# Kernel tuning notes

Hardware: AMD Instinct MI355X
Metric: run time of the kernel (lower is better)

The kernel has to match this reference:

```python
import jax, jax.numpy as jnp
import numpy as np

N, E, B = 50000, 800000, 1000
NODE_DIN, BB_DOUT, DHID, K = 32, 64, 64, 3
GLOB_DIN, EMBED_DIN = 64, 64
CIN = BB_DOUT + NODE_DIN  # 96


def setup_inputs() -> dict:
    key = jax.random.key(0)
    ks = jax.random.split(key, 24)

    def w(k, shape, fan_in):
        return jax.random.normal(k, shape, jnp.float32) / np.float32(np.sqrt(fan_in))

    inp = dict(
        x=jax.random.normal(ks[0], (N, NODE_DIN), jnp.float32),
        u=jax.random.normal(ks[1], (B, GLOB_DIN), jnp.float32),
        z=jax.random.normal(ks[2], (N, BB_DOUT), jnp.float32),
        edge_index=jax.random.randint(ks[3], (2, E), 0, N),
        edge_weight=jax.random.uniform(ks[4], (E,), jnp.float32),
        batch=jnp.sort(jax.random.randint(ks[5], (N,), 0, B)),
        batch_size=B,
        prev_h=jax.random.normal(ks[6], (N, DHID), jnp.float32),
    )
    # six ChebConvs of GConvGRU: x-convs take CIN, h-convs take DHID; all output DHID
    for i, nm in enumerate(["xz", "hz", "xr", "hr", "xh", "hh"]):
        cin = CIN if nm[0] == "x" else DHID
        inp[f"W{nm}"] = w(ks[7 + 2 * i], (K, cin, DHID), cin * K)
        inp[f"b{nm}"] = jnp.zeros((DHID,), jnp.float32)
    inp["Wg"] = w(ks[20], (GLOB_DIN, EMBED_DIN), GLOB_DIN)
    inp["bg"] = jnp.zeros((EMBED_DIN,), jnp.float32)
    return inp


def _cheb(xin, W, b, src, dst, w_norm, n):
    """ChebConv with sym norm, lambda_max=2 -> L_hat = -D^-1/2 A D^-1/2 (diag cancels)."""
    def prop(t):  # L_hat @ t  ([N,C])
        return -jax.ops.segment_sum(w_norm[:, None] * t[src], dst, num_segments=n)

    out = xin @ W[0] + b
    tx_prev = xin
    tx = None
    if W.shape[0] > 1:
        tx = prop(xin)
        out = out + tx @ W[1]
    for k in range(2, W.shape[0]):
        tx_new = 2.0 * prop(tx) - tx_prev
        out = out + tx_new @ W[k]
        tx_prev, tx = tx, tx_new
    return out


def reference(x, u, z, edge_index, edge_weight, batch, batch_size, prev_h,
              Wxz, bxz, Whz, bhz, Wxr, bxr, Whr, bhr, Wxh, bxh, Whh, bhh, Wg, bg):
    n = x.shape[0]
    src, dst = edge_index[0], edge_index[1]
    deg = jax.ops.segment_sum(edge_weight, src, num_segments=n)
    deg_safe = jnp.where(deg > 0, deg, 1.0)
    dinv = jnp.where(deg > 0, jax.lax.rsqrt(deg_safe), 0.0)
    w_norm = dinv[src] * edge_weight * dinv[dst]

    xin = jnp.concatenate([z, x], axis=-1)  # [N, CIN]
    Z = jax.nn.sigmoid(_cheb(xin, Wxz, bxz, src, dst, w_norm, n)
                       + _cheb(prev_h, Whz, bhz, src, dst, w_norm, n))
    R = jax.nn.sigmoid(_cheb(xin, Wxr, bxr, src, dst, w_norm, n)
                       + _cheb(prev_h, Whr, bhr, src, dst, w_norm, n))
    Ht = jnp.tanh(_cheb(xin, Wxh, bxh, src, dst, w_norm, n)
                  + _cheb(prev_h * R, Whh, bhh, src, dst, w_norm, n))
    h = Z * prev_h + (1.0 - Z) * Ht

    graph_emb = jax.ops.segment_sum(z, batch, num_segments=batch_size)  # [B, BB_DOUT]
    global_emb = jax.nn.relu(u @ Wg + bg)                                # [B, EMBED_DIN]
    fused = jnp.concatenate([graph_emb, global_emb], axis=-1)           # [B, 128]
    return fused, h
```

## Files before the change

### kernel.cpp

```cpp
#include <hip/hip_runtime.h>

#define NN 50000
#define EE 800000
#define BB 1000
#define NB 196
#define NR 8
#define RS 6272
#define NC 32
#define CHUNK 25000

#define DEGBLKS (NR * NC)
#define BUILDBLKS 15625
#define PACKBLKS 204

typedef unsigned short u16;
typedef __attribute__((ext_vector_type(8))) short bf16x8;
typedef __attribute__((ext_vector_type(4))) float f32x4;

static __device__ __forceinline__ u16 f2b(float f) {
    union { float f; unsigned u; } v;
    v.f = f;
    unsigned r = v.u + 0x7fffu + ((v.u >> 16) & 1u);
    return (u16)(r >> 16);
}

static __device__ __forceinline__ float b2f(short s) {
    union { unsigned u; float f; } c;
    c.u = ((unsigned)(u16)s) << 16;
    return c.f;
}

__global__ __launch_bounds__(512) void k_front(
    const int* __restrict__ src, const int* __restrict__ dst,
    const float* __restrict__ ew, float* __restrict__ deg_p, int* __restrict__ cnt_p,
    const float* __restrict__ z, const float* __restrict__ x,
    const float* __restrict__ ph, u16* __restrict__ A,
    const float* __restrict__ Wxz, const float* __restrict__ Wxr,
    const float* __restrict__ Wxh, const float* __restrict__ Whz,
    const float* __restrict__ Whr, const float* __restrict__ Whh,
    u16* __restrict__ Wp, u16* __restrict__ W3p, int* __restrict__ ctr) {
    __shared__ float sdeg[RS];
    __shared__ int scnt[RS];
    int bid = blockIdx.x;
    if (bid < DEGBLKS) {
        if (bid == 0 && threadIdx.x == 0) atomicExch(ctr, 0);
        int r = bid & (NR - 1);
        int c = bid >> 3;
        int base = r * RS;
        for (int i = threadIdx.x; i < RS; i += 512) {
            sdeg[i] = 0.f;
            scnt[i] = 0;
        }
        __syncthreads();
        int e0 = c * CHUNK;
        for (int j = threadIdx.x; j < CHUNK; j += 512) {
            int e = e0 + j;
            int s = src[e], d = dst[e];
            int sl = s - base, dl = d - base;
            if ((unsigned)sl < RS) atomicAdd(&sdeg[sl], ew[e]);
            if ((unsigned)dl < RS) atomicAdd(&scnt[dl], 1);
        }
        __syncthreads();
        int lim = (NN - base < RS) ? (NN - base) : RS;
        for (int i = threadIdx.x; i < lim; i += 512) {
            deg_p[(size_t)c * NN + base + i] = sdeg[i];
            cnt_p[(size_t)c * NN + base + i] = scnt[i];
        }
    } else if (bid < DEGBLKS + BUILDBLKS) {
        int i = (bid - DEGBLKS) * 512 + threadIdx.x;
        int n = i / 160, c = i - n * 160;
        float v;
        if (c < 64) v = z[n * 64 + c];
        else if (c < 96) v = x[n * 32 + (c - 64)];
        else v = ph[n * 64 + (c - 96)];
        A[(size_t)n * 480 + c] = f2b(v);
    } else {
        int idx = (bid - DEGBLKS - BUILDBLKS) * 512 + threadIdx.x;
        if (idx < 15 * 12 * 512) {
            int j = idx & 7, l = (idx >> 3) & 63;
            int ct = (idx >> 9) % 12, s = (idx >> 9) / 12;
            int k = 32 * s + (l >> 4) * 8 + j;
            int g = ct >> 2;
            int c = 16 * (ct & 3) + (l & 15);
            bool isX;
            int kr;
            if (k < 96)       { isX = true;  kr = k; }
            else if (k < 160) { isX = false; kr = k - 96; }
            else if (k < 256) { isX = true;  kr = 96 + (k - 160); }
            else if (k < 320) { isX = false; kr = 64 + (k - 256); }
            else if (k < 416) { isX = true;  kr = 192 + (k - 320); }
            else              { isX = false; kr = 128 + (k - 416); }
            float val;
            if (isX) {
                const float* W = (g == 0) ? Wxz : ((g == 1) ? Wxr : Wxh);
                val = W[kr * 64 + c];
            } else if (g == 2) {
                val = 0.f;
            } else {
                const float* W = (g == 0) ? Whz : Whr;
                val = W[kr * 64 + c];
            }
            Wp[idx] = f2b(val);
        } else {
            int i2 = idx - 15 * 12 * 512;
            int j = i2 & 7, l = (i2 >> 3) & 63;
            int ct = (i2 >> 9) & 3, s = i2 >> 11;
            int k = 32 * s + (l >> 4) * 8 + j;
            int ki = k >> 6, kr = k & 63;
            int c = 16 * ct + (l & 15);
            W3p[i2] = f2b(Whh[(ki * 64 + kr) * 64 + c]);
        }
    }
}

__global__ __launch_bounds__(256) void k_scan(
    const int* __restrict__ cnt_p, const float* __restrict__ deg_p,
    int* __restrict__ cnt, int* __restrict__ row_ptr, int* __restrict__ cursor,
    float* __restrict__ dinv, int* __restrict__ bsum, int* __restrict__ ctr) {
    __shared__ int s[256];
    int b = blockIdx.x;
    int i = b * 256 + threadIdx.x;
    int v = 0;
    float d = 0.f;
    if (i < NN) {
#pragma unroll
        for (int p = 0; p < NC; p++) v += cnt_p[(size_t)p * NN + i];
#pragma unroll
        for (int p = 0; p < NC; p++) d += deg_p[(size_t)p * NN + i];
        cnt[i] = v;
    }
    s[threadIdx.x] = v;
    __syncthreads();
    for (int off = 1; off < 256; off <<= 1) {
        int t = (threadIdx.x >= off) ? s[threadIdx.x - off] : 0;
        __syncthreads();
        s[threadIdx.x] += t;
        __syncthreads();
    }
    int incl = s[threadIdx.x];
    if (threadIdx.x == 255) atomicExch(&bsum[b], s[255]);
    __threadfence();
    if (threadIdx.x == 0) {
        atomicAdd(ctr, 1);
        while (atomicAdd(ctr, 0) < NB) __builtin_amdgcn_s_sleep(8);
    }
    __syncthreads();
    __threadfence();
    int pv = (threadIdx.x < b) ? atomicAdd(&bsum[threadIdx.x], 0) : 0;
    s[threadIdx.x] = pv;
    __syncthreads();
    for (int off = 128; off > 0; off >>= 1) {
        if (threadIdx.x < off) s[threadIdx.x] += s[threadIdx.x + off];
        __syncthreads();
    }
    int prefix = s[0];
    if (i < NN) {
        int start = prefix + incl - v;
        row_ptr[i] = start;
        cursor[i] = start;
        dinv[i] = d > 0.f ? rsqrtf(d) : 0.f;
    }
}

__global__ void k_scatter(const int* __restrict__ src, const int* __restrict__ dst,
                          const float* __restrict__ ew, const float* __restrict__ dinv,
                          int* __restrict__ cursor, uint2* __restrict__ csr8) {
    int e = blockIdx.x * 256 + threadIdx.x;
    if (e >= EE) return;
    int d = dst[e], s = src[e];
    int pos = atomicAdd(&cursor[d], 1);
    float w = dinv[s] * ew[e] * dinv[d];
    csr8[pos] = make_uint2((unsigned)s, __float_as_uint(w));
}

template <int C, int SCALE, bool HB, int BS, int OS>
__global__ __launch_bounds__(BS) void k_pull(
    const u16* __restrict__ Abase, int inofs, int baseofs, int outofs,
    const uint2* __restrict__ csr8, const int* __restrict__ row_ptr,
    const int* __restrict__ cnt) {
    constexpr int TPR = C / 16;
    int tid = blockIdx.x * BS + threadIdx.x;
    int r = tid / TPR;
    int c16 = (tid - r * TPR) * 16;
    if (r >= NN) return;
    int s0 = row_ptr[r], n = cnt[r];
    float acc[16];
#pragma unroll
    for (int k = 0; k < 16; k++) acc[k] = 0.f;
    const u16* in = Abase + inofs + c16;
    uint2 e = (n > 0) ? csr8[s0] : make_uint2(0u, 0u);
    for (int j = 0; j < n; j++) {
        uint2 ec = e;
        if (j + 1 < n) e = csr8[s0 + j + 1];
        float w = __uint_as_float(ec.y);
        const u16* p = in + (size_t)ec.x * OS;
        bf16x8 v0 = *(const bf16x8*)(p);
        bf16x8 v1 = *(const bf16x8*)(p + 8);
#pragma unroll
        for (int k = 0; k < 8; k++) {
            acc[k] += w * b2f(v0[k]);
            acc[8 + k] += w * b2f(v1[k]);
        }
    }
    const float sc = -(float)SCALE;
    float o[16];
    if (HB) {
        const u16* bp = Abase + (size_t)r * OS + baseofs + c16;
        bf16x8 b0 = *(const bf16x8*)(bp);
        bf16x8 b1 = *(const bf16x8*)(bp + 8);
#pragma unroll
        for (int k = 0; k < 8; k++) {
            o[k] = sc * acc[k] - b2f(b0[k]);
            o[8 + k] = sc * acc[8 + k] - b2f(b1[k]);
        }
    } else {
#pragma unroll
        for (int k = 0; k < 16; k++) o[k] = sc * acc[k];
    }
    bf16x8 p0, p1;
#pragma unroll
    for (int k = 0; k < 8; k++) {
        p0[k] = (short)f2b(o[k]);
        p1[k] = (short)f2b(o[8 + k]);
    }
    u16* op = const_cast<u16*>(Abase) + (size_t)r * OS + outofs + c16;
    *(bf16x8*)(op) = p0;
    *(bf16x8*)(op + 8) = p1;
}

__global__ __launch_bounds__(256) void k_gates_mfma(
    const u16* __restrict__ A, const u16* __restrict__ Wp,
    const float* __restrict__ bxz, const float* __restrict__ bhz,
    const float* __restrict__ bxr, const float* __restrict__ bhr,
    const float* __restrict__ bxh,
    u16* __restrict__ Zb16, u16* __restrict__ Hx16, u16* __restrict__ A3) {
    int wv = (blockIdx.x * 256 + threadIdx.x) >> 6;
    int lane = threadIdx.x & 63;
    int r0 = wv * 16;
    if (r0 >= NN) return;
    int q = lane >> 4, j0 = lane & 15;

    f32x4 acc[12];
#pragma unroll
    for (int i = 0; i < 12; i++) acc[i] = (f32x4){0.f, 0.f, 0.f, 0.f};

    const u16* arow = A + (size_t)(r0 + j0) * 480 + q * 8;
#pragma unroll
    for (int s = 0; s < 15; s++) {
        bf16x8 a = *(const bf16x8*)(arow + 32 * s);
        const u16* bp = Wp + (size_t)(s * 12) * 512 + lane * 8;
#pragma unroll
        for (int ct = 0; ct < 12; ct++) {
            bf16x8 b = *(const bf16x8*)(bp + ct * 512);
            acc[ct] = __builtin_amdgcn_mfma_f32_16x16x32_bf16(a, b, acc[ct], 0, 0, 0);
        }
    }

#pragma unroll
    for (int ct = 0; ct < 4; ct++) {
        int j = 16 * ct + j0;
        float bz = bxz[j] + bhz[j];
        float br = bxr[j] + bhr[j];
        float bh = bxh[j];
#pragma unroll
        for (int reg = 0; reg < 4; reg++) {
            int r = r0 + q * 4 + reg;
            size_t i = (size_t)r * 64 + j;
            float zp = acc[ct][reg] + bz;
            float rp = acc[ct + 4][reg] + br;
            float hp = acc[ct + 8][reg] + bh;
            float zv = 1.f / (1.f + expf(-zp));
            float rv = 1.f / (1.f + expf(-rp));
            float phv = b2f((short)A[(size_t)r * 480 + 96 + j]);
            Zb16[i] = f2b(zv);
            Hx16[i] = f2b(hp);
            A3[(size_t)r * 192 + j] = f2b(rv * phv);
        }
    }
}

#define FINBLKS 782
__global__ __launch_bounds__(256) void k_final_tail(
    const u16* __restrict__ A3, const u16* __restrict__ W3p,
    const float* __restrict__ bhh, const u16* __restrict__ Hx16,
    const u16* __restrict__ Zb16, const u16* __restrict__ A,
    float* __restrict__ outh,
    const float* __restrict__ z, const int* __restrict__ batch,
    const float* __restrict__ u, const float* __restrict__ Wg,
    const float* __restrict__ bg, float* __restrict__ outF) {
    if (blockIdx.x >= FINBLKS) {
        int b = ((blockIdx.x - FINBLKS) * 256 + threadIdx.x) >> 6;
        int lane = threadIdx.x & 63;
        if (b >= BB) return;
        int lo = 0, hi = NN;
        while (lo < hi) {
            int m = (lo + hi) >> 1;
            if (batch[m] < b) lo = m + 1; else hi = m;
        }
        int start = lo;
        hi = NN;
        while (lo < hi) {
            int m = (lo + hi) >> 1;
            if (batch[m] < b + 1) lo = m + 1; else hi = m;
        }
        int end = lo;
        float acc = 0.f;
        for (int n = start; n < end; n++) acc += z[(size_t)n * 64 + lane];
        float g = bg[lane];
        const float* ur = u + (size_t)b * 64;
        for (int k = 0; k < 64; k++) g += ur[k] * Wg[k * 64 + lane];
        g = fmaxf(g, 0.f);
        outF[(size_t)b * 128 + lane] = acc;
        outF[(size_t)b * 128 + 64 + lane] = g;
        return;
    }
    int wv = (blockIdx.x * 256 + threadIdx.x) >> 6;
    int lane = threadIdx.x & 63;
    int r0 = wv * 16;
    if (r0 >= NN) return;
    int q = lane >> 4, j0 = lane & 15;

    f32x4 acc[4];
#pragma unroll
    for (int i = 0; i < 4; i++) acc[i] = (f32x4){0.f, 0.f, 0.f, 0.f};

    const u16* arow = A3 + (size_t)(r0 + j0) * 192 + q * 8;
#pragma unroll
    for (int s = 0; s < 6; s++) {
        bf16x8 a = *(const bf16x8*)(arow + 32 * s);
        const u16* bp = W3p + (size_t)(s * 4) * 512 + lane * 8;
#pragma unroll
        for (int ct = 0; ct < 4; ct++) {
            bf16x8 b = *(const bf16x8*)(bp + ct * 512);
            acc[ct] = __builtin_amdgcn_mfma_f32_16x16x32_bf16(a, b, acc[ct], 0, 0, 0);
        }
    }

#pragma unroll
    for (int ct = 0; ct < 4; ct++) {
        int j = 16 * ct + j0;
        float bh = bhh[j];
#pragma unroll
        for (int reg = 0; reg < 4; reg++) {
            int r = r0 + q * 4 + reg;
            size_t i = (size_t)r * 64 + j;
            float ht = tanhf(b2f((short)Hx16[i]) + acc[ct][reg] + bh);
            float zv = b2f((short)Zb16[i]);
            float phv = b2f((short)A[(size_t)r * 480 + 96 + j]);
            outh[i] = zv * phv + (1.f - zv) * ht;
        }
    }
}

extern "C" void kernel_launch(void* const* d_in, const int* in_sizes, int n_in,
                              void* d_out, int out_size, void* d_ws, size_t ws_size,
                              hipStream_t stream) {
    const float* x  = (const float*)d_in[0];
    const float* u  = (const float*)d_in[1];
    const float* z  = (const float*)d_in[2];
    const int*   ei = (const int*)d_in[3];
    const float* ew = (const float*)d_in[4];
    const int* batch = (const int*)d_in[5];
    const float* ph = (const float*)d_in[7];
    const float *Wxz = (const float*)d_in[8],  *bxz = (const float*)d_in[9];
    const float *Whz = (const float*)d_in[10], *bhz = (const float*)d_in[11];
    const float *Wxr = (const float*)d_in[12], *bxr = (const float*)d_in[13];
    const float *Whr = (const float*)d_in[14], *bhr = (const float*)d_in[15];
    const float *Wxh = (const float*)d_in[16], *bxh = (const float*)d_in[17];
    const float *Whh = (const float*)d_in[18], *bhh = (const float*)d_in[19];
    const float *Wg  = (const float*)d_in[20], *bg  = (const float*)d_in[21];
    const int* src = ei;
    const int* dst = ei + EE;

    char* wsb = (char*)d_ws;
    size_t o = 0;
    auto alloc = [&](size_t bytes) {
        void* p = wsb + o;
        o += (bytes + 255) & ~(size_t)255;
        return p;
    };
    float* deg_p   = (float*)alloc((size_t)NC * NN * 4);
    int*   cnt_p   = (int*)alloc((size_t)NC * NN * 4);
    int*   cnt     = (int*)alloc(NN * 4);
    int*   row_ptr = (int*)alloc(NN * 4);
    int*   cursor  = (int*)alloc(NN * 4);
    float* dinv    = (float*)alloc(NN * 4);
    int*   bsum    = (int*)alloc(256 * 4);
    int*   ctr     = (int*)alloc(256);
    uint2* csr8    = (uint2*)alloc((size_t)EE * 8);
    u16*   Zb16 = (u16*)alloc((size_t)NN * 64 * 2);
    u16*   Hx16 = (u16*)alloc((size_t)NN * 64 * 2);
    u16*   A    = (u16*)alloc((size_t)NN * 480 * 2);
    u16*   A3   = (u16*)alloc((size_t)NN * 192 * 2);
    u16*   Wp   = (u16*)alloc(15 * 12 * 512 * 2);
    u16*   W3p  = (u16*)alloc(6 * 4 * 512 * 2);

    float* outF = (float*)d_out;
    float* outH = outF + (size_t)BB * 128;

    const int BLK = 256;
    const int gE = (EE + BLK - 1) / BLK;
    const int gPull160 = (NN + 31) / 32;
    const int gPull64 = (NN + 63) / 64;
    const int gMFMA = FINBLKS;
    const int gTail = (BB * 64 + BLK - 1) / BLK;

    k_front<<<DEGBLKS + BUILDBLKS + PACKBLKS, 512, 0, stream>>>(
        src, dst, ew, deg_p, cnt_p, z, x, ph, A,
        Wxz, Wxr, Wxh, Whz, Whr, Whh, Wp, W3p, ctr);

    k_scan<<<NB, 256, 0, stream>>>(cnt_p, deg_p, cnt, row_ptr, cursor, dinv, bsum, ctr);

    k_scatter<<<gE, BLK, 0, stream>>>(src, dst, ew, dinv, cursor, csr8);

    k_pull<160, 1, false, 320, 480><<<gPull160, 320, 0, stream>>>(A, 0, 0, 160, csr8, row_ptr, cnt);
    k_pull<160, 2, true, 320, 480><<<gPull160, 320, 0, stream>>>(A, 160, 0, 320, csr8, row_ptr, cnt);

    k_gates_mfma<<<gMFMA, BLK, 0, stream>>>(A, Wp, bxz, bhz, bxr, bhr, bxh, Zb16, Hx16, A3);

    k_pull<64, 1, false, 256, 192><<<gPull64, 256, 0, stream>>>(A3, 0, 0, 64, csr8, row_ptr, cnt);
    k_pull<64, 2, true, 256, 192><<<gPull64, 256, 0, stream>>>(A3, 64, 0, 128, csr8, row_ptr, cnt);

    k_final_tail<<<gMFMA + gTail, BLK, 0, stream>>>(A3, W3p, bhh, Hx16, Zb16, A, outH,
                                                    z, batch, u, Wg, bg, outF);
}
```

Measured before the change: 426.6 us.

## Replace atomic CSR scatter with per-chunk rank scatter and split A buffer

The CSR build no longer uses global atomic cursors. A histogram pass packs 16-bit destination counts in shared memory over 5 row ranges. The scan now also produces per-chunk base offsets, and a new scatter kernel ranks edges with shared-memory atomics and writes them deterministically. The interleaved 480-wide A buffer is split into three 160-wide buffers, and the feature/weight packing moves into the scan launch. The aim is to cut global atomic contention during the scatter, at the cost of a 32xN cbase array and a second pass over the edges.

```diff
diff --git a/kernel.cpp b/kernel.cpp
--- a/kernel.cpp
+++ b/kernel.cpp
@@ -4,14 +4,14 @@
 #define EE 800000
 #define BB 1000
 #define NB 196
-#define NR 8
-#define RS 6272
+#define NR 5
+#define RS 10496
 #define NC 32
 #define CHUNK 25000
 
-#define DEGBLKS (NR * NC)
-#define BUILDBLKS 15625
-#define PACKBLKS 204
+#define BUILD2 31250
+#define PACK2 408
+#define FINBLKS 782
 
 typedef unsigned short u16;
 typedef __attribute__((ext_vector_type(8))) short bf16x8;
@@ -30,93 +30,87 @@
     return c.f;
 }
 
-__global__ __launch_bounds__(512) void k_front(
+__global__ __launch_bounds__(512) void k_hist(
     const int* __restrict__ src, const int* __restrict__ dst,
-    const float* __restrict__ ew, float* __restrict__ deg_p, int* __restrict__ cnt_p,
+    const float* __restrict__ ew, float* __restrict__ deg_p,
+    int* __restrict__ cnt_p, int* __restrict__ ctr) {
+    __shared__ float sdeg[RS];
+    __shared__ unsigned scnt2[RS / 2];
+    if (blockIdx.x == 0 && threadIdx.x == 0) atomicExch(ctr, 0);
+    int r = blockIdx.x % NR;
+    int c = blockIdx.x / NR;
+    int base = r * RS;
+    for (int i = threadIdx.x; i < RS; i += 512) sdeg[i] = 0.f;
+    for (int i = threadIdx.x; i < RS / 2; i += 512) scnt2[i] = 0u;
+    __syncthreads();
+    int e0 = c * CHUNK;
+    for (int j = threadIdx.x; j < CHUNK; j += 512) {
+        int e = e0 + j;
+        int s = src[e], d = dst[e];
+        int sl = s - base, dl = d - base;
+        if ((unsigned)sl < RS) atomicAdd(&sdeg[sl], ew[e]);
+        if ((unsigned)dl < RS) atomicAdd(&scnt2[dl >> 1], (dl & 1) ? 65536u : 1u);
+    }
+    __syncthreads();
+    int lim = (NN - base < RS) ? (NN - base) : RS;
+    for (int i = threadIdx.x; i < lim; i += 512) {
+        deg_p[(size_t)c * NN + base + i] = sdeg[i];
+        cnt_p[(size_t)c * NN + base + i] = (int)((scnt2[i >> 1] >> ((i & 1) * 16)) & 0xffffu);
+    }
+}
+
+__global__ __launch_bounds__(256) void k_scan_build(
+    const int* __restrict__ cnt_p, const float* __restrict__ deg_p,
+    int* __restrict__ cnt, int* __restrict__ cbase, float* __restrict__ dinv,
+    int* __restrict__ bsum, int* __restrict__ ctr,
     const float* __restrict__ z, const float* __restrict__ x,
-    const float* __restrict__ ph, u16* __restrict__ A,
+    const float* __restrict__ ph, u16* __restrict__ A0,
     const float* __restrict__ Wxz, const float* __restrict__ Wxr,
     const float* __restrict__ Wxh, const float* __restrict__ Whz,
     const float* __restrict__ Whr, const float* __restrict__ Whh,
-    u16* __restrict__ Wp, u16* __restrict__ W3p, int* __restrict__ ctr) {
-    __shared__ float sdeg[RS];
-    __shared__ int scnt[RS];
-    int bid = blockIdx.x;
-    if (bid < DEGBLKS) {
-        if (bid == 0 && threadIdx.x == 0) atomicExch(ctr, 0);
-        int r = bid & (NR - 1);
-        int c = bid >> 3;
-        int base = r * RS;
-        for (int i = threadIdx.x; i < RS; i += 512) {
-            sdeg[i] = 0.f;
-            scnt[i] = 0;
-        }
-        __syncthreads();
-        int e0 = c * CHUNK;
-        for (int j = threadIdx.x; j < CHUNK; j += 512) {
-            int e = e0 + j;
-            int s = src[e], d = dst[e];
-            int sl = s - base, dl = d - base;
-            if ((unsigned)sl < RS) atomicAdd(&sdeg[sl], ew[e]);
-            if ((unsigned)dl < RS) atomicAdd(&scnt[dl], 1);
-        }
-        __syncthreads();
-        int lim = (NN - base < RS) ? (NN - base) : RS;
-        for (int i = threadIdx.x; i < lim; i += 512) {
-            deg_p[(size_t)c * NN + base + i] = sdeg[i];
-            cnt_p[(size_t)c * NN + base + i] = scnt[i];
-        }
-    } else if (bid < DEGBLKS + BUILDBLKS) {
-        int i = (bid - DEGBLKS) * 512 + threadIdx.x;
-        int n = i / 160, c = i - n * 160;
-        float v;
-        if (c < 64) v = z[n * 64 + c];
-        else if (c < 96) v = x[n * 32 + (c - 64)];
-        else v = ph[n * 64 + (c - 96)];
-        A[(size_t)n * 480 + c] = f2b(v);
-    } else {
-        int idx = (bid - DEGBLKS - BUILDBLKS) * 512 + threadIdx.x;
-        if (idx < 15 * 12 * 512) {
-            int j = idx & 7, l = (idx >> 3) & 63;
-            int ct = (idx >> 9) % 12, s = (idx >> 9) / 12;
-            int k = 32 * s + (l >> 4) * 8 + j;
-            int g = ct >> 2;
-            int c = 16 * (ct & 3) + (l & 15);
-            bool isX;
-            int kr;
-            if (k < 96)       { isX = true;  kr = k; }
-            else if (k < 160) { isX = false; kr = k - 96; }
-            else if (k < 256) { isX = true;  kr = 96 + (k - 160); }
-            else if (k < 320) { isX = false; kr = 64 + (k - 256); }
-            else if (k < 416) { isX = true;  kr = 192 + (k - 320); }
-            else              { isX = false; kr = 128 + (k - 416); }
-            float val;
-            if (isX) {
-                const float* W = (g == 0) ? Wxz : ((g == 1) ? Wxr : Wxh);
-                val = W[kr * 64 + c];
-            } else if (g == 2) {
-                val = 0.f;
+    u16* __restrict__ Wp, u16* __restrict__ W3p) {
+    if (blockIdx.x >= NB) {
+        int bid = blockIdx.x - NB;
+        if (bid < BUILD2) {
+            int i = bid * 256 + threadIdx.x;
+            int n = i / 160, c = i - n * 160;
+            float v;
+            if (c < 64) v = z[n * 64 + c];
+            else if (c < 96) v = x[n * 32 + (c - 64)];
+            else v = ph[n * 64 + (c - 96)];
+            A0[(size_t)n * 160 + c] = f2b(v);
+        } else {
+            int idx = (bid - BUILD2) * 256 + threadIdx.x;
+            if (idx < 15 * 12 * 512) {
+                int j = idx & 7, l = (idx >> 3) & 63;
+                int ct = (idx >> 9) % 12, s = (idx >> 9) / 12;
+                int k = 32 * s + (l >> 4) * 8 + j;
+                int g = ct >> 2;
+                int c = 16 * (ct & 3) + (l & 15);
+                int lvl = k / 160, kk = k - lvl * 160;
+                float val;
+                if (kk < 96) {
+                    const float* W = (g == 0) ? Wxz : ((g == 1) ? Wxr : Wxh);
+                    val = W[(lvl * 96 + kk) * 64 + c];
+                } else if (g == 2) {
+                    val = 0.f;
+                } else {
+                    const float* W = (g == 0) ? Whz : Whr;
+                    val = W[(lvl * 64 + (kk - 96)) * 64 + c];
+                }
+                Wp[idx] = f2b(val);
             } else {
-                const float* W = (g == 0) ? Whz : Whr;
-                val = W[kr * 64 + c];
+                int i2 = idx - 15 * 12 * 512;
+                int j = i2 & 7, l = (i2 >> 3) & 63;
+                int ct = (i2 >> 9) & 3, s = i2 >> 11;
+                int k = 32 * s + (l >> 4) * 8 + j;
+                int ki = k >> 6, kr = k & 63;
+                int c = 16 * ct + (l & 15);
+                W3p[i2] = f2b(Whh[(ki * 64 + kr) * 64 + c]);
             }
-            Wp[idx] = f2b(val);
-        } else {
-            int i2 = idx - 15 * 12 * 512;
-            int j = i2 & 7, l = (i2 >> 3) & 63;
-            int ct = (i2 >> 9) & 3, s = i2 >> 11;
-            int k = 32 * s + (l >> 4) * 8 + j;
-            int ki = k >> 6, kr = k & 63;
-            int c = 16 * ct + (l & 15);
-            W3p[i2] = f2b(Whh[(ki * 64 + kr) * 64 + c]);
-        }
-    }
-}
-
-__global__ __launch_bounds__(256) void k_scan(
-    const int* __restrict__ cnt_p, const float* __restrict__ deg_p,
-    int* __restrict__ cnt, int* __restrict__ row_ptr, int* __restrict__ cursor,
-    float* __restrict__ dinv, int* __restrict__ bsum, int* __restrict__ ctr) {
+        }
+        return;
+    }
     __shared__ int s[256];
     int b = blockIdx.x;
     int i = b * 256 + threadIdx.x;
@@ -155,27 +149,45 @@
     }
     int prefix = s[0];
     if (i < NN) {
-        int start = prefix + incl - v;
-        row_ptr[i] = start;
-        cursor[i] = start;
+        int run = prefix + incl - v;
         dinv[i] = d > 0.f ? rsqrtf(d) : 0.f;
-    }
-}
-
-__global__ void k_scatter(const int* __restrict__ src, const int* __restrict__ dst,
-                          const float* __restrict__ ew, const float* __restrict__ dinv,
-                          int* __restrict__ cursor, uint2* __restrict__ csr8) {
-    int e = blockIdx.x * 256 + threadIdx.x;
-    if (e >= EE) return;
-    int d = dst[e], s = src[e];
-    int pos = atomicAdd(&cursor[d], 1);
-    float w = dinv[s] * ew[e] * dinv[d];
-    csr8[pos] = make_uint2((unsigned)s, __float_as_uint(w));
-}
-
-template <int C, int SCALE, bool HB, int BS, int OS>
+#pragma unroll
+        for (int c = 0; c < NC; c++) {
+            cbase[(size_t)c * NN + i] = run;
+            run += cnt_p[(size_t)c * NN + i];
+        }
+    }
+}
+
+__global__ __launch_bounds__(512) void k_scatter_rank(
+    const int* __restrict__ src, const int* __restrict__ dst,
+    const float* __restrict__ ew, const float* __restrict__ dinv,
+    const int* __restrict__ cbase, uint2* __restrict__ csr8) {
+    __shared__ unsigned rank2[RS / 2];
+    int r = blockIdx.x % NR;
+    int c = blockIdx.x / NR;
+    int base = r * RS;
+    for (int i = threadIdx.x; i < RS / 2; i += 512) rank2[i] = 0u;
+    __syncthreads();
+    int e0 = c * CHUNK;
+    for (int j = threadIdx.x; j < CHUNK; j += 512) {
+        int e = e0 + j;
+        int d = dst[e];
+        int dl = d - base;
+        if ((unsigned)dl < RS) {
+            int s = src[e];
+            unsigned old = atomicAdd(&rank2[dl >> 1], (dl & 1) ? 65536u : 1u);
+            int rank = (int)((old >> ((dl & 1) * 16)) & 0xffffu);
+            int pos = cbase[(size_t)c * NN + d] + rank;
+            float w = dinv[s] * ew[e] * dinv[d];
+            csr8[pos] = make_uint2((unsigned)s, __float_as_uint(w));
+        }
+    }
+}
+
+template <int C, int SCALE, bool HB, int BS, int INS, int OUTS>
 __global__ __launch_bounds__(BS) void k_pull(
-    const u16* __restrict__ Abase, int inofs, int baseofs, int outofs,
+    const u16* __restrict__ in, const u16* __restrict__ base, u16* __restrict__ out,
     const uint2* __restrict__ csr8, const int* __restrict__ row_ptr,
     const int* __restrict__ cnt) {
     constexpr int TPR = C / 16;
@@ -187,13 +199,13 @@
     float acc[16];
 #pragma unroll
     for (int k = 0; k < 16; k++) acc[k] = 0.f;
-    const u16* in = Abase + inofs + c16;
+    const u16* inp = in + c16;
     uint2 e = (n > 0) ? csr8[s0] : make_uint2(0u, 0u);
     for (int j = 0; j < n; j++) {
         uint2 ec = e;
         if (j + 1 < n) e = csr8[s0 + j + 1];
         float w = __uint_as_float(ec.y);
-        const u16* p = in + (size_t)ec.x * OS;
+        const u16* p = inp + (size_t)ec.x * INS;
         bf16x8 v0 = *(const bf16x8*)(p);
         bf16x8 v1 = *(const bf16x8*)(p + 8);
 #pragma unroll
@@ -205,7 +217,7 @@
     const float sc = -(float)SCALE;
     float o[16];
     if (HB) {
-        const u16* bp = Abase + (size_t)r * OS + baseofs + c16;
+        const u16* bp = base + (size_t)r * INS + c16;
         bf16x8 b0 = *(const bf16x8*)(bp);
         bf16x8 b1 = *(const bf16x8*)(bp + 8);
 #pragma unroll
@@ -223,13 +235,14 @@
         p0[k] = (short)f2b(o[k]);
         p1[k] = (short)f2b(o[8 + k]);
     }
-    u16* op = const_cast<u16*>(Abase) + (size_t)r * OS + outofs + c16;
+    u16* op = out + (size_t)r * OUTS + c16;
     *(bf16x8*)(op) = p0;
     *(bf16x8*)(op + 8) = p1;
 }
 
 __global__ __launch_bounds__(256) void k_gates_mfma(
-    const u16* __restrict__ A, const u16* __restrict__ Wp,
+    const u16* __restrict__ A0, const u16* __restrict__ A1, const u16* __restrict__ A2,
+    const u16* __restrict__ Wp,
     const float* __restrict__ bxz, const float* __restrict__ bhz,
     const float* __restrict__ bxr, const float* __restrict__ bhr,
     const float* __restrict__ bxh,
@@ -244,10 +257,11 @@
 #pragma unroll
     for (int i = 0; i < 12; i++) acc[i] = (f32x4){0.f, 0.f, 0.f, 0.f};
 
-    const u16* arow = A + (size_t)(r0 + j0) * 480 + q * 8;
+    size_t rofs = (size_t)(r0 + j0) * 160 + q * 8;
+    const u16* arow[3] = {A0 + rofs, A1 + rofs, A2 + rofs};
 #pragma unroll
     for (int s = 0; s < 15; s++) {
-        bf16x8 a = *(const bf16x8*)(arow + 32 * s);
+        bf16x8 a = *(const bf16x8*)(arow[s / 5] + 32 * (s % 5));
         const u16* bp = Wp + (size_t)(s * 12) * 512 + lane * 8;
 #pragma unroll
         for (int ct = 0; ct < 12; ct++) {
@@ -271,7 +285,7 @@
             float hp = acc[ct + 8][reg] + bh;
             float zv = 1.f / (1.f + expf(-zp));
             float rv = 1.f / (1.f + expf(-rp));
-            float phv = b2f((short)A[(size_t)r * 480 + 96 + j]);
+            float phv = b2f((short)A0[(size_t)r * 160 + 96 + j]);
             Zb16[i] = f2b(zv);
             Hx16[i] = f2b(hp);
             A3[(size_t)r * 192 + j] = f2b(rv * phv);
@@ -279,11 +293,10 @@
     }
 }
 
-#define FINBLKS 782
 __global__ __launch_bounds__(256) void k_final_tail(
     const u16* __restrict__ A3, const u16* __restrict__ W3p,
     const float* __restrict__ bhh, const u16* __restrict__ Hx16,
-    const u16* __restrict__ Zb16, const u16* __restrict__ A,
+    const u16* __restrict__ Zb16, const u16* __restrict__ A0,
     float* __restrict__ outh,
     const float* __restrict__ z, const int* __restrict__ batch,
     const float* __restrict__ u, const float* __restrict__ Wg,
@@ -346,7 +359,7 @@
             size_t i = (size_t)r * 64 + j;
             float ht = tanhf(b2f((short)Hx16[i]) + acc[ct][reg] + bh);
             float zv = b2f((short)Zb16[i]);
-            float phv = b2f((short)A[(size_t)r * 480 + 96 + j]);
+            float phv = b2f((short)A0[(size_t)r * 160 + 96 + j]);
             outh[i] = zv * phv + (1.f - zv) * ht;
         }
     }
@@ -379,48 +392,53 @@
         o += (bytes + 255) & ~(size_t)255;
         return p;
     };
-    float* deg_p   = (float*)alloc((size_t)NC * NN * 4);
-    int*   cnt_p   = (int*)alloc((size_t)NC * NN * 4);
-    int*   cnt     = (int*)alloc(NN * 4);
-    int*   row_ptr = (int*)alloc(NN * 4);
-    int*   cursor  = (int*)alloc(NN * 4);
-    float* dinv    = (float*)alloc(NN * 4);
-    int*   bsum    = (int*)alloc(256 * 4);
-    int*   ctr     = (int*)alloc(256);
-    uint2* csr8    = (uint2*)alloc((size_t)EE * 8);
-    u16*   Zb16 = (u16*)alloc((size_t)NN * 64 * 2);
-    u16*   Hx16 = (u16*)alloc((size_t)NN * 64 * 2);
-    u16*   A    = (u16*)alloc((size_t)NN * 480 * 2);
-    u16*   A3   = (u16*)alloc((size_t)NN * 192 * 2);
-    u16*   Wp   = (u16*)alloc(15 * 12 * 512 * 2);
-    u16*   W3p  = (u16*)alloc(6 * 4 * 512 * 2);
+    float* deg_p = (float*)alloc((size_t)NC * NN * 4);
+    int*   cnt_p = (int*)alloc((size_t)NC * NN * 4);
+    int*   cnt   = (int*)alloc(NN * 4);
+    int*   cbase = (int*)alloc((size_t)NC * NN * 4);
+    float* dinv  = (float*)alloc(NN * 4);
+    int*   bsum  = (int*)alloc(256 * 4);
+    int*   ctr   = (int*)alloc(256);
+    uint2* csr8  = (uint2*)alloc((size_t)EE * 8);
+    u16*   Zb16  = (u16*)alloc((size_t)NN * 64 * 2);
+    u16*   Hx16  = (u16*)alloc((size_t)NN * 64 * 2);
+    u16*   A0    = (u16*)alloc((size_t)NN * 160 * 2);
+    u16*   A1    = (u16*)alloc((size_t)NN * 160 * 2);
+    u16*   A2    = (u16*)alloc((size_t)NN * 160 * 2);
+    u16*   A3    = (u16*)alloc((size_t)NN * 192 * 2);
+    u16*   Wp    = (u16*)alloc(15 * 12 * 512 * 2);
+    u16*   W3p   = (u16*)alloc(6 * 4 * 512 * 2);
 
     float* outF = (float*)d_out;
     float* outH = outF + (size_t)BB * 128;
 
     const int BLK = 256;
-    const int gE = (EE + BLK - 1) / BLK;
     const int gPull160 = (NN + 31) / 32;
     const int gPull64 = (NN + 63) / 64;
-    const int gMFMA = FINBLKS;
     const int gTail = (BB * 64 + BLK - 1) / BLK;
-
-    k_front<<<DEGBLKS + BUILDBLKS + PACKBLKS, 512, 0, stream>>>(
-        src, dst, ew, deg_p, cnt_p, z, x, ph, A,
-        Wxz, Wxr, Wxh, Whz, Whr, Whh, Wp, W3p, ctr);
-
-    k_scan<<<NB, 256, 0, stream>>>(cnt_p, deg_p, cnt, row_ptr, cursor, dinv, bsum, ctr);
-
-    k_scatter<<<gE, BLK, 0, stream>>>(src, dst, ew, dinv, cursor, csr8);
-
-    k_pull<160, 1, false, 320, 480><<<gPull160, 320, 0, stream>>>(A, 0, 0, 160, csr8, row_ptr, cnt);
-    k_pull<160, 2, true, 320, 480><<<gPull160, 320, 0, stream>>>(A, 160, 0, 320, csr8, row_ptr, cnt);
-
-    k_gates_mfma<<<gMFMA, BLK, 0, stream>>>(A, Wp, bxz, bhz, bxr, bhr, bxh, Zb16, Hx16, A3);
-
-    k_pull<64, 1, false, 256, 192><<<gPull64, 256, 0, stream>>>(A3, 0, 0, 64, csr8, row_ptr, cnt);
-    k_pull<64, 2, true, 256, 192><<<gPull64, 256, 0, stream>>>(A3, 64, 0, 128, csr8, row_ptr, cnt);
-
-    k_final_tail<<<gMFMA + gTail, BLK, 0, stream>>>(A3, W3p, bhh, Hx16, Zb16, A, outH,
-                                                    z, batch, u, Wg, bg, outF);
-}
+    int* row_ptr = cbase;
+
+    k_hist<<<NR * NC, 512, 0, stream>>>(src, dst, ew, deg_p, cnt_p, ctr);
+
+    k_scan_build<<<NB + BUILD2 + PACK2, 256, 0, stream>>>(
+        cnt_p, deg_p, cnt, cbase, dinv, bsum, ctr,
+        z, x, ph, A0, Wxz, Wxr, Wxh, Whz, Whr, Whh, Wp, W3p);
+
+    k_scatter_rank<<<NR * NC, 512, 0, stream>>>(src, dst, ew, dinv, cbase, csr8);
+
+    k_pull<160, 1, false, 320, 160, 160><<<gPull160, 320, 0, stream>>>(
+        A0, nullptr, A1, csr8, row_ptr, cnt);
+    k_pull<160, 2, true, 320, 160, 160><<<gPull160, 320, 0, stream>>>(
+        A1, A0, A2, csr8, row_ptr, cnt);
+
+    k_gates_mfma<<<FINBLKS, BLK, 0, stream>>>(A0, A1, A2, Wp, bxz, bhz, bxr, bhr, bxh,
+                                              Zb16, Hx16, A3);
+
+    k_pull<64, 1, false, 256, 192, 192><<<gPull64, 256, 0, stream>>>(
+        A3, nullptr, A3 + 64, csr8, row_ptr, cnt);
+    k_pull<64, 2, true, 256, 192, 192><<<gPull64, 256, 0, stream>>>(
+        A3 + 64, A3, A3 + 128, csr8, row_ptr, cnt);
+
+    k_final_tail<<<FINBLKS + gTail, BLK, 0, stream>>>(A3, W3p, bhh, Hx16, Zb16, A0, outH,
+                                                      z, batch, u, Wg, bg, outF);
+}
```

After: 458.3 us. +7.4%, slower.
